# Performance work log

Measured on AMD Instinct MI355X. Metric: run time of the kernel, lower is better.

## Reference

```python
import jax, jax.numpy as jnp
import numpy as np
import math

VOCAB = 2048
SEQ = 2048
BATCH = 8
NEG_INF = -1e30


def setup_inputs() -> dict:
    key = jax.random.key(0)
    ks = jax.random.split(key, 8)
    sV = 1.0 / math.sqrt(VOCAB)
    sS = 1.0 / math.sqrt(SEQ)
    return {
        "input": jax.random.randint(ks[0], (BATCH, SEQ), 0, VOCAB),
        "emb": jax.random.normal(ks[1], (VOCAB, VOCAB), jnp.float32),   # nn.Embedding(vocab, vocab)
        "pos": jax.random.normal(ks[2], (SEQ, SEQ), jnp.float32),       # nn.Embedding(seq, seq)
        "WQ1": jax.random.normal(ks[3], (SEQ, SEQ), jnp.float32) * sS,  # Linear(seq, seq), (out,in)
        "WK1": jax.random.normal(ks[4], (SEQ, SEQ), jnp.float32) * sS,
        "WV1": jax.random.normal(ks[5], (VOCAB, VOCAB), jnp.float32) * sV,
        "WQ2": jax.random.normal(ks[6], (VOCAB, VOCAB), jnp.float32) * sV,
        "WK2": jax.random.normal(ks[7], (VOCAB, VOCAB), jnp.float32) * sV,
        "beta_1": jnp.float32(1.0),
        "beta_2": jnp.float32(1.0),
        "beta_out": jnp.float32(1.0),
    }


def reference(input, emb, pos, WQ1, WK1, WV1, WQ2, WK2, beta_1, beta_2, beta_out):
    S, V = SEQ, VOCAB
    E = emb[input]                       # (B, S, V)
    P = pos                              # positions(arange(S)) == full table, (S, S)

    # --- stage 1: batch-independent causal attention over positions ---
    Q1 = P @ WQ1.T                       # (S, S)
    K1 = P @ WK1.T                       # (S, S)
    S1 = beta_1 * (Q1 @ K1.T) / math.sqrt(S)
    causal = jnp.tril(jnp.ones((S, S), bool))
    S1 = jnp.where(causal, S1, NEG_INF)
    A1 = jax.nn.softmax(S1, axis=-1)
    A1 = A1.at[0, :].set(0.0)            # zero first query row (per-batch identical)

    V1 = jnp.einsum('bsv,wv->bsw', E, WV1)   # WV1(E), (B, S, V)
    Y1 = jnp.einsum('st,btv->bsv', A1, V1)
    Z1 = E + Y1                          # (B, S, V)

    # --- stage 2: single-query attention ---
    q2 = Z1[:, -1] @ WQ2.T               # (B, V)
    K2 = jnp.einsum('bsv,wv->bsw', Z1, WK2)  # (B, S, V)
    S2 = beta_2 * jnp.einsum('bv,bsv->bs', q2, K2) / math.sqrt(V)  # (B, S)
    last_two = jnp.arange(S) >= S - 2
    S2 = jnp.where(last_two[None, :], NEG_INF, S2)
    A2 = jax.nn.softmax(S2, axis=-1)     # (B, S)

    Y2 = jnp.einsum('bs,bsv->bv', A2, E)
    return beta_out * Y2                 # (B, V) == output[:, 0, :]
```

## Files before the change

kernel.cpp:

```cpp
#include <hip/hip_runtime.h>
#include <math.h>

#define SEQ 2048
#define VOCAB 2048
#define BATCH 8
#define NTRIL 136

typedef unsigned short u16;
typedef __attribute__((ext_vector_type(4))) float f32x4;
typedef __attribute__((ext_vector_type(8))) short bf16x8;

__device__ __forceinline__ u16 f2bf(float f) {
  unsigned int u = __builtin_bit_cast(unsigned int, f);
  u += 0x7fffu + ((u >> 16) & 1u);
  return (u16)(u >> 16);
}

__device__ __forceinline__ float b2f(u16 h) {
  unsigned int u = ((unsigned int)h) << 16;
  return __builtin_bit_cast(float, u);
}

__device__ __forceinline__ void async16(const void* g, void* l) {
  __builtin_amdgcn_global_load_lds((const __attribute__((address_space(1))) void*)g,
                                   (__attribute__((address_space(3))) void*)l, 16, 0, 0);
}

__global__ __launch_bounds__(256) void cvt_all(const float* __restrict__ pos, const float* __restrict__ WQ1,
                                               const float* __restrict__ WK1, u16* __restrict__ Pbf,
                                               u16* __restrict__ Wqk, float4* __restrict__ zreg, int nz4) {
  const int i = blockIdx.x * 256 + threadIdx.x;
  const int seg = blockIdx.y;
  if (seg == 3) {
    if (i < nz4) zreg[i] = make_float4(0.f, 0.f, 0.f, 0.f);
    return;
  }
  const float* src = (seg == 0) ? pos : (seg == 1) ? WQ1 : WK1;
  u16* dst = (seg == 0) ? Pbf : (seg == 1) ? Wqk : Wqk + (size_t)SEQ * SEQ;
  float4 v = ((const float4*)src)[i];
  ushort4 o;
  o.x = f2bf(v.x); o.y = f2bf(v.y); o.z = f2bf(v.z); o.w = f2bf(v.w);
  ((ushort4*)dst)[i] = o;
}

__device__ __forceinline__ void stage_tile(const u16* __restrict__ A, const u16* __restrict__ B,
                                           u16* As, u16* Bs, int m0, int n0, int kt,
                                           int wid, int lane) {
  const int c0 = wid * 2;
  const int skel = (lane & 3) * 8;
#pragma unroll
  for (int r = 0; r < 2; ++r) {
    const int chunk = c0 + r;
    const int row = chunk * 16 + (lane >> 2);
    async16(A + (size_t)(m0 + row) * SEQ + kt + skel, As + chunk * 512);
    async16(B + (size_t)(n0 + row) * SEQ + kt + skel, Bs + chunk * 512);
  }
}

__device__ __forceinline__ void compute_tile(const u16* As, const u16* Bs, f32x4 acc[4][4],
                                             int wr, int wc, int frow, int fk) {
  bf16x8 af[4], bfv[4];
#pragma unroll
  for (int mi = 0; mi < 4; ++mi) af[mi] = *(const bf16x8*)&As[(wr * 64 + mi * 16 + frow) * 32 + fk];
#pragma unroll
  for (int ni = 0; ni < 4; ++ni) bfv[ni] = *(const bf16x8*)&Bs[(wc * 64 + ni * 16 + frow) * 32 + fk];
#pragma unroll
  for (int mi = 0; mi < 4; ++mi)
#pragma unroll
    for (int ni = 0; ni < 4; ++ni)
      acc[mi][ni] = __builtin_amdgcn_mfma_f32_16x16x32_bf16(af[mi], bfv[ni], acc[mi][ni], 0, 0, 0);
}

__global__ __launch_bounds__(256) void gemm_qk(const u16* __restrict__ A, const u16* __restrict__ Bw,
                                               u16* __restrict__ Q1b, u16* __restrict__ K1b) {
  __shared__ __align__(16) u16 As0[4096], Bs0[4096], As1[4096], Bs1[4096];
  const int bid = blockIdx.x;
  const int xcd = bid & 7, li = bid >> 3;
  const int tx = (xcd & 3) * 8 + (li & 7);
  const int ty = (xcd >> 2) * 8 + (li >> 3);
  const int m0 = ty * 128;
  const int n0 = tx * 128;

  const int tid = threadIdx.x;
  const int wid = tid >> 6;
  const int lane = tid & 63;
  const int wr = wid >> 1, wc = wid & 1;
  const int frow = lane & 15;
  const int fk = (lane >> 4) * 8;

  f32x4 acc[4][4];
#pragma unroll
  for (int i = 0; i < 4; ++i)
#pragma unroll
    for (int j = 0; j < 4; ++j) acc[i][j] = (f32x4){0.f, 0.f, 0.f, 0.f};

  stage_tile(A, Bw, As0, Bs0, m0, n0, 0, wid, lane);
  __syncthreads();
  const int NT = SEQ / 32;
  for (int t = 0; t < NT - 1; t += 2) {
    stage_tile(A, Bw, As1, Bs1, m0, n0, (t + 1) * 32, wid, lane);
    compute_tile(As0, Bs0, acc, wr, wc, frow, fk);
    __syncthreads();
    if (t + 2 < NT) stage_tile(A, Bw, As0, Bs0, m0, n0, (t + 2) * 32, wid, lane);
    compute_tile(As1, Bs1, acc, wr, wc, frow, fk);
    __syncthreads();
  }

  u16* outp = (n0 < SEQ) ? Q1b : K1b;
  const int rbase = m0 + wr * 64;
  const int cbase = (n0 < SEQ ? n0 : n0 - SEQ) + wc * 64;
  const int rl = (lane >> 4) * 4;
  const int cl = lane & 15;
#pragma unroll
  for (int mi = 0; mi < 4; ++mi)
#pragma unroll
    for (int ni = 0; ni < 4; ++ni)
#pragma unroll
      for (int i = 0; i < 4; ++i) {
        int rr = rbase + mi * 16 + rl + i;
        int cc = cbase + ni * 16 + cl;
        outp[(size_t)rr * SEQ + cc] = f2bf(acc[mi][ni][i]);
      }
}

__global__ __launch_bounds__(256) void gemm_s1(const u16* __restrict__ A, const u16* __restrict__ B,
                                               u16* __restrict__ part) {
  __shared__ __align__(16) u16 As0[4096], Bs0[4096], As1[4096], Bs1[4096];
  const int bid = blockIdx.x;
  const int split = bid & 3;
  const int t = bid >> 2;
  int ti_m = 0;
  while (((ti_m + 1) * (ti_m + 2)) / 2 <= t) ++ti_m;
  const int ti_n = t - (ti_m * (ti_m + 1)) / 2;
  const int m0 = ti_m * 128;
  const int n0 = ti_n * 128;
  const int kt0 = split * (SEQ / 4);

  const int tid = threadIdx.x;
  const int wid = tid >> 6;
  const int lane = tid & 63;
  const int wr = wid >> 1, wc = wid & 1;
  const int frow = lane & 15;
  const int fk = (lane >> 4) * 8;

  f32x4 acc[4][4];
#pragma unroll
  for (int i = 0; i < 4; ++i)
#pragma unroll
    for (int j = 0; j < 4; ++j) acc[i][j] = (f32x4){0.f, 0.f, 0.f, 0.f};

  stage_tile(A, B, As0, Bs0, m0, n0, kt0, wid, lane);
  __syncthreads();
  const int NT = (SEQ / 4) / 32;
  for (int tt = 0; tt < NT - 1; tt += 2) {
    stage_tile(A, B, As1, Bs1, m0, n0, kt0 + (tt + 1) * 32, wid, lane);
    compute_tile(As0, Bs0, acc, wr, wc, frow, fk);
    __syncthreads();
    if (tt + 2 < NT) stage_tile(A, B, As0, Bs0, m0, n0, kt0 + (tt + 2) * 32, wid, lane);
    compute_tile(As1, Bs1, acc, wr, wc, frow, fk);
    __syncthreads();
  }

  u16* dst = part + ((size_t)(split * NTRIL + t) << 14);
  const int rb = wr * 64;
  const int cb = wc * 64;
  const int rl = (lane >> 4) * 4;
  const int cl = lane & 15;
#pragma unroll
  for (int mi = 0; mi < 4; ++mi)
#pragma unroll
    for (int ni = 0; ni < 4; ++ni)
#pragma unroll
      for (int i = 0; i < 4; ++i)
        dst[(rb + mi * 16 + rl + i) * 128 + (cb + ni * 16 + cl)] = f2bf(acc[mi][ni][i]);
}

__global__ __launch_bounds__(256) void softmax_last(const u16* __restrict__ part, const float* __restrict__ b1p,
                                                    const int* __restrict__ idx, float* __restrict__ cnt1) {
  const int b = blockIdx.x;
  const int tid = threadIdx.x, lane = tid & 63, w = tid >> 6;
  __shared__ float buf[SEQ];
  __shared__ float red[8];
  const float c1 = b1p[0] / sqrtf((float)SEQ);
  const int base_t = 120;
  const u16* p0 = part + ((size_t)(0 * NTRIL + base_t) << 14) + 127 * 128;
  const u16* p1 = part + ((size_t)(1 * NTRIL + base_t) << 14) + 127 * 128;
  const u16* p2 = part + ((size_t)(2 * NTRIL + base_t) << 14) + 127 * 128;
  const u16* p3 = part + ((size_t)(3 * NTRIL + base_t) << 14) + 127 * 128;
  float mx = -3.0e38f;
  for (int q = tid; q < SEQ / 4; q += 256) {
    const size_t o = ((size_t)(q >> 5) << 14) + ((q << 2) & 127);
    ushort4 a0 = *(const ushort4*)(p0 + o);
    ushort4 a1 = *(const ushort4*)(p1 + o);
    ushort4 a2 = *(const ushort4*)(p2 + o);
    ushort4 a3 = *(const ushort4*)(p3 + o);
    float v0 = (b2f(a0.x) + b2f(a1.x) + b2f(a2.x) + b2f(a3.x)) * c1;
    float v1 = (b2f(a0.y) + b2f(a1.y) + b2f(a2.y) + b2f(a3.y)) * c1;
    float v2 = (b2f(a0.z) + b2f(a1.z) + b2f(a2.z) + b2f(a3.z)) * c1;
    float v3 = (b2f(a0.w) + b2f(a1.w) + b2f(a2.w) + b2f(a3.w)) * c1;
    const int j = q << 2;
    buf[j] = v0; buf[j + 1] = v1; buf[j + 2] = v2; buf[j + 3] = v3;
    mx = fmaxf(mx, fmaxf(fmaxf(v0, v1), fmaxf(v2, v3)));
  }
  for (int o = 32; o > 0; o >>= 1) mx = fmaxf(mx, __shfl_down(mx, o));
  if (lane == 0) red[w] = mx;
  __syncthreads();
  if (tid == 0) { float m = red[0]; for (int i = 1; i < 4; ++i) m = fmaxf(m, red[i]); red[4] = m; }
  __syncthreads();
  const float MX = red[4];
  float sm = 0.f;
  for (int j = tid; j < SEQ; j += 256) {
    float e = expf(buf[j] - MX);
    buf[j] = e;
    sm += e;
  }
  for (int o = 32; o > 0; o >>= 1) sm += __shfl_down(sm, o);
  if (lane == 0) red[w] = sm;
  __syncthreads();
  if (tid == 0) { float tt = 0.f; for (int i = 0; i < 4; ++i) tt += red[i]; red[5] = tt; }
  __syncthreads();
  const float inv = 1.0f / red[5];
  for (int j = tid; j < SEQ; j += 256)
    atomicAdd(&cnt1[b * VOCAB + idx[b * SEQ + j]], buf[j] * inv);
}

__global__ __launch_bounds__(256) void matvec_col(const float* __restrict__ M, const float* __restrict__ x,
                                                  float* __restrict__ outp, const float* __restrict__ scale_ptr) {
  const int vb = blockIdx.x * 256 + threadIdx.x;
  const int w0 = blockIdx.y * 32;
  __shared__ float xs[BATCH][32];
  { int k = threadIdx.x; xs[k >> 5][k & 31] = x[(k >> 5) * VOCAB + w0 + (k & 31)]; }
  __syncthreads();
  float acc[BATCH];
#pragma unroll
  for (int b = 0; b < BATCH; ++b) acc[b] = 0.f;
#pragma unroll 8
  for (int j = 0; j < 32; ++j) {
    float m = M[(size_t)(w0 + j) * VOCAB + vb];
#pragma unroll
    for (int b = 0; b < BATCH; ++b) acc[b] += xs[b][j] * m;
  }
  float sc = scale_ptr ? scale_ptr[0] : 1.0f;
#pragma unroll
  for (int b = 0; b < BATCH; ++b) atomicAdd(&outp[b * VOCAB + vb], sc * acc[b]);
}

template<int GATHER_ADD>
__global__ __launch_bounds__(256) void matvec_row(const float* __restrict__ M, const float* __restrict__ x,
                                                  float* __restrict__ outp, const int* __restrict__ idx,
                                                  const float* __restrict__ emb) {
  const int lane = threadIdx.x & 63;
  const int i = blockIdx.x * 4 + (threadIdx.x >> 6);
  const float4* m4 = (const float4*)(M + (size_t)i * VOCAB);
  const float4* x4 = (const float4*)x;
  float acc[BATCH];
#pragma unroll
  for (int b = 0; b < BATCH; ++b) acc[b] = 0.f;
  for (int v = lane; v < VOCAB / 4; v += 64) {
    float4 m = m4[v];
#pragma unroll
    for (int b = 0; b < BATCH; ++b) {
      float4 xv = x4[b * (VOCAB / 4) + v];
      acc[b] += m.x * xv.x + m.y * xv.y + m.z * xv.z + m.w * xv.w;
    }
  }
#pragma unroll
  for (int b = 0; b < BATCH; ++b)
    for (int o = 32; o > 0; o >>= 1) acc[b] += __shfl_down(acc[b], o);
  if (lane == 0) {
#pragma unroll
    for (int b = 0; b < BATCH; ++b) {
      float s = acc[b];
      if (GATHER_ADD) s += emb[(size_t)idx[b * SEQ + SEQ - 1] * VOCAB + i];
      outp[b * VOCAB + i] = s;
    }
  }
}

__global__ __launch_bounds__(256) void emb_dots16(const float* __restrict__ emb, const float* __restrict__ rw,
                                                  float* __restrict__ D) {
  const int lane = threadIdx.x & 63;
  const int i = blockIdx.x * 4 + (threadIdx.x >> 6);
  const float4* e4 = (const float4*)(emb + (size_t)i * VOCAB);
  const float4* r4 = (const float4*)rw;
  float acc[16];
#pragma unroll
  for (int j = 0; j < 16; ++j) acc[j] = 0.f;
  for (int v = lane; v < VOCAB / 4; v += 64) {
    float4 m = e4[v];
#pragma unroll
    for (int j = 0; j < 16; ++j) {
      float4 r = r4[j * (VOCAB / 4) + v];
      acc[j] += m.x * r.x + m.y * r.y + m.z * r.z + m.w * r.w;
    }
  }
#pragma unroll
  for (int j = 0; j < 16; ++j)
    for (int o = 32; o > 0; o >>= 1) acc[j] += __shfl_down(acc[j], o);
  if (lane == 0) {
#pragma unroll
    for (int j = 0; j < 16; ++j) D[(size_t)i * 16 + j] = acc[j];
  }
}

__global__ __launch_bounds__(256) void gath_u(const int* __restrict__ idx, const float* __restrict__ D,
                                              float* __restrict__ u) {
  const int i = blockIdx.x * 256 + threadIdx.x;
  const int b = i >> 11;
  u[i] = D[(size_t)idx[i] * 16 + 8 + b];
}

__global__ __launch_bounds__(256) void sm_apply(const u16* __restrict__ part, const float* __restrict__ b1p,
                                                const float* __restrict__ u, float* __restrict__ vv) {
  const int s = blockIdx.x;
  const int tid = threadIdx.x, lane = tid & 63, w = tid >> 6;
  if (s == 0) {
    if (tid < BATCH) vv[tid * SEQ] = 0.f;
    return;
  }
  __shared__ float buf[SEQ];
  __shared__ float red[8];
  __shared__ float red2[4][BATCH];
  const float c1 = b1p[0] / sqrtf((float)SEQ);
  const int base_t = (s >> 7) * ((s >> 7) + 1) / 2;
  const int rloc = (s & 127) * 128;
  const u16* p0 = part + ((size_t)(0 * NTRIL + base_t) << 14) + rloc;
  const u16* p1 = part + ((size_t)(1 * NTRIL + base_t) << 14) + rloc;
  const u16* p2 = part + ((size_t)(2 * NTRIL + base_t) << 14) + rloc;
  const u16* p3 = part + ((size_t)(3 * NTRIL + base_t) << 14) + rloc;
  float mx = -3.0e38f;
  const int nq = (s + 1) >> 2;
  for (int q = tid; q < nq; q += 256) {
    const size_t o = ((size_t)(q >> 5) << 14) + ((q << 2) & 127);
    ushort4 a0 = *(const ushort4*)(p0 + o);
    ushort4 a1 = *(const ushort4*)(p1 + o);
    ushort4 a2 = *(const ushort4*)(p2 + o);
    ushort4 a3 = *(const ushort4*)(p3 + o);
    float v0 = (b2f(a0.x) + b2f(a1.x) + b2f(a2.x) + b2f(a3.x)) * c1;
    float v1 = (b2f(a0.y) + b2f(a1.y) + b2f(a2.y) + b2f(a3.y)) * c1;
    float v2 = (b2f(a0.z) + b2f(a1.z) + b2f(a2.z) + b2f(a3.z)) * c1;
    float v3 = (b2f(a0.w) + b2f(a1.w) + b2f(a2.w) + b2f(a3.w)) * c1;
    const int j = q << 2;
    buf[j] = v0; buf[j + 1] = v1; buf[j + 2] = v2; buf[j + 3] = v3;
    mx = fmaxf(mx, fmaxf(fmaxf(v0, v1), fmaxf(v2, v3)));
  }
  {
    const int j = (nq << 2) + tid;
    if (j <= s) {
      const size_t o = ((size_t)(j >> 7) << 14) + (j & 127);
      float v = (b2f(p0[o]) + b2f(p1[o]) + b2f(p2[o]) + b2f(p3[o])) * c1;
      buf[j] = v;
      mx = fmaxf(mx, v);
    }
  }
  for (int o = 32; o > 0; o >>= 1) mx = fmaxf(mx, __shfl_down(mx, o));
  if (lane == 0) red[w] = mx;
  __syncthreads();
  if (tid == 0) { float m = red[0]; for (int i = 1; i < 4; ++i) m = fmaxf(m, red[i]); red[4] = m; }
  __syncthreads();
  const float MX = red[4];
  float sm = 0.f;
  for (int j = tid; j <= s; j += 256) {
    float e = expf(buf[j] - MX);
    buf[j] = e;
    sm += e;
  }
  for (int o = 32; o > 0; o >>= 1) sm += __shfl_down(sm, o);
  if (lane == 0) red[w] = sm;
  __syncthreads();
  if (tid == 0) { float tt = 0.f; for (int i = 0; i < 4; ++i) tt += red[i]; red[5] = tt; }
  __syncthreads();
  const float inv = 1.0f / red[5];
  float acc[BATCH];
#pragma unroll
  for (int b = 0; b < BATCH; ++b) acc[b] = 0.f;
  for (int q = tid; q < nq; q += 256) {
    const int j = q << 2;
    float4 a = *(float4*)&buf[j];
#pragma unroll
    for (int b = 0; b < BATCH; ++b) {
      float4 uv = *(const float4*)(u + b * SEQ + j);
      acc[b] += a.x * uv.x + a.y * uv.y + a.z * uv.z + a.w * uv.w;
    }
  }
  {
    const int j = (nq << 2) + tid;
    if (j <= s) {
      float a = buf[j];
#pragma unroll
      for (int b = 0; b < BATCH; ++b) acc[b] += a * u[b * SEQ + j];
    }
  }
#pragma unroll
  for (int b = 0; b < BATCH; ++b)
    for (int o = 32; o > 0; o >>= 1) acc[b] += __shfl_down(acc[b], o);
  if (lane == 0)
#pragma unroll
    for (int b = 0; b < BATCH; ++b) red2[w][b] = acc[b];
  __syncthreads();
  if (tid < BATCH)
    vv[tid * SEQ + s] = (red2[0][tid] + red2[1][tid] + red2[2][tid] + red2[3][tid]) * inv;
}

__global__ __launch_bounds__(256) void softmax2(const float* __restrict__ D, const float* __restrict__ vv,
                                                const int* __restrict__ idx, float* __restrict__ cnt2,
                                                const float* __restrict__ b2p, float4* __restrict__ out_zero) {
  const int b = blockIdx.x;
  const int tid = threadIdx.x, lane = tid & 63, w = tid >> 6;
  for (int k = b * 256 + tid; k < BATCH * VOCAB / 4; k += BATCH * 256)
    out_zero[k] = make_float4(0.f, 0.f, 0.f, 0.f);
  __shared__ float buf[SEQ];
  __shared__ float red[8];
  const float c2 = b2p[0] / sqrtf((float)VOCAB);
  for (int s = tid; s < SEQ; s += 256) {
    float val = -1.0e30f;
    if (s < SEQ - 2) {
      float ee = D[(size_t)idx[b * SEQ + s] * 16 + b];
      val = c2 * (ee + vv[b * SEQ + s]);
    }
    buf[s] = val;
  }
  __syncthreads();
  float mx = -3.0e38f;
  for (int s = tid; s < SEQ; s += 256) mx = fmaxf(mx, buf[s]);
  for (int o = 32; o > 0; o >>= 1) mx = fmaxf(mx, __shfl_down(mx, o));
  if (lane == 0) red[w] = mx;
  __syncthreads();
  if (tid == 0) { float m = red[0]; for (int i = 1; i < 4; ++i) m = fmaxf(m, red[i]); red[4] = m; }
  __syncthreads();
  const float MX = red[4];
  float sm = 0.f;
  for (int s = tid; s < SEQ; s += 256) {
    float e = expf(buf[s] - MX);
    buf[s] = e;
    sm += e;
  }
  for (int o = 32; o > 0; o >>= 1) sm += __shfl_down(sm, o);
  if (lane == 0) red[w] = sm;
  __syncthreads();
  if (tid == 0) { float tt = 0.f; for (int i = 0; i < 4; ++i) tt += red[i]; red[5] = tt; }
  __syncthreads();
  const float inv = 1.0f / red[5];
  for (int s = tid; s < SEQ - 2; s += 256)
    atomicAdd(&cnt2[b * VOCAB + idx[b * SEQ + s]], buf[s] * inv);
}

extern "C" void kernel_launch(void* const* d_in, const int* in_sizes, int n_in,
                              void* d_out, int out_size, void* d_ws, size_t ws_size,
                              hipStream_t stream) {
  (void)in_sizes; (void)n_in; (void)out_size; (void)ws_size;
  const int*   idx = (const int*)d_in[0];
  const float* emb = (const float*)d_in[1];
  const float* pos = (const float*)d_in[2];
  const float* WQ1 = (const float*)d_in[3];
  const float* WK1 = (const float*)d_in[4];
  const float* WV1 = (const float*)d_in[5];
  const float* WQ2 = (const float*)d_in[6];
  const float* WK2 = (const float*)d_in[7];
  const float* b1  = (const float*)d_in[8];
  const float* b2  = (const float*)d_in[9];
  const float* bo  = (const float*)d_in[10];
  float* out = (float*)d_out;

  size_t off = 0;
  auto take = [&](size_t n) { void* p = (char*)d_ws + off; off += (n + 255) & ~(size_t)255; return p; };
  u16*   Pbf  = (u16*)take((size_t)SEQ * SEQ * 2);
  u16*   Wqk  = (u16*)take((size_t)SEQ * SEQ * 4);
  u16*   Q1b  = (u16*)take((size_t)SEQ * SEQ * 2);
  u16*   K1b  = (u16*)take((size_t)SEQ * SEQ * 2);
  u16*   S1p  = (u16*)take((size_t)4 * NTRIL * 16384 * 2);
  float* g    = (float*)take((size_t)BATCH * VOCAB * 4);
  float* cnt1 = (float*)take((size_t)BATCH * VOCAB * 4);
  float* rr   = (float*)take((size_t)BATCH * VOCAB * 4);
  float* wv   = (float*)take((size_t)BATCH * VOCAB * 4);
  float* cnt2 = (float*)take((size_t)BATCH * VOCAB * 4);
  float* zl   = (float*)take((size_t)BATCH * VOCAB * 4);
  float* q2   = (float*)take((size_t)BATCH * VOCAB * 4);
  float* D    = (float*)take((size_t)VOCAB * 16 * 4);
  float* uu   = (float*)take((size_t)BATCH * SEQ * 4);
  float* vv   = (float*)take((size_t)BATCH * SEQ * 4);
  (void)wv;

  const int nz4 = 5 * BATCH * VOCAB / 4;

  cvt_all<<<dim3(SEQ * SEQ / 4 / 256, 4), 256, 0, stream>>>(pos, WQ1, WK1, Pbf, Wqk, (float4*)g, nz4);

  gemm_qk<<<512, 256, 0, stream>>>(Pbf, Wqk, Q1b, K1b);

  gemm_s1<<<4 * NTRIL, 256, 0, stream>>>(Q1b, K1b, S1p);

  softmax_last<<<BATCH, 256, 0, stream>>>(S1p, b1, idx, cnt1);

  matvec_col<<<dim3(VOCAB / 256, 64), 256, 0, stream>>>(emb, cnt1, g, nullptr);

  matvec_row<1><<<VOCAB / 4, 256, 0, stream>>>(WV1, g, zl, idx, emb);
  matvec_row<0><<<VOCAB / 4, 256, 0, stream>>>(WQ2, zl, q2, nullptr, nullptr);

  matvec_col<<<dim3(VOCAB / 256, 64), 256, 0, stream>>>(WK2, q2, rr, nullptr);
  matvec_col<<<dim3(VOCAB / 256, 64), 256, 0, stream>>>(WV1, rr, wv, nullptr);

  emb_dots16<<<VOCAB / 4, 256, 0, stream>>>(emb, rr, D);

  gath_u<<<BATCH * SEQ / 256, 256, 0, stream>>>(idx, D, uu);

  sm_apply<<<SEQ, 256, 0, stream>>>(S1p, b1, uu, vv);

  softmax2<<<BATCH, 256, 0, stream>>>(D, vv, idx, cnt2, b2, (float4*)out);

  matvec_col<<<dim3(VOCAB / 256, 64), 256, 0, stream>>>(emb, cnt2, out, bo);
}
```

Baseline: 162.4 us.

## Deepen GEMM K-tile to 64 and compute four emb rows per wave

The two bf16 GEMMs now stage and compute 64-wide K slices per double-buffer step instead of 32, which halves the number of barriers and loop iterations and doubles LDS use per block. emb_dots16 now has each wave process four embedding rows, so every rw vector loaded is reused four times, and the grid shrinks to a quarter. The risks are lower occupancy from the larger LDS footprint, the 64-entry accumulator array raising register pressure, and far fewer blocks in emb_dots16.

```diff
diff --git a/kernel.cpp b/kernel.cpp
--- a/kernel.cpp
+++ b/kernel.cpp
@@ -43,37 +43,45 @@
   ((ushort4*)dst)[i] = o;
 }
 
-__device__ __forceinline__ void stage_tile(const u16* __restrict__ A, const u16* __restrict__ B,
-                                           u16* As, u16* Bs, int m0, int n0, int kt,
-                                           int wid, int lane) {
+__device__ __forceinline__ void stage64(const u16* __restrict__ A, const u16* __restrict__ B,
+                                        u16* As, u16* Bs, int m0, int n0, int kt,
+                                        int wid, int lane) {
   const int c0 = wid * 2;
   const int skel = (lane & 3) * 8;
 #pragma unroll
   for (int r = 0; r < 2; ++r) {
     const int chunk = c0 + r;
     const int row = chunk * 16 + (lane >> 2);
-    async16(A + (size_t)(m0 + row) * SEQ + kt + skel, As + chunk * 512);
-    async16(B + (size_t)(n0 + row) * SEQ + kt + skel, Bs + chunk * 512);
-  }
-}
-
-__device__ __forceinline__ void compute_tile(const u16* As, const u16* Bs, f32x4 acc[4][4],
-                                             int wr, int wc, int frow, int fk) {
-  bf16x8 af[4], bfv[4];
-#pragma unroll
-  for (int mi = 0; mi < 4; ++mi) af[mi] = *(const bf16x8*)&As[(wr * 64 + mi * 16 + frow) * 32 + fk];
-#pragma unroll
-  for (int ni = 0; ni < 4; ++ni) bfv[ni] = *(const bf16x8*)&Bs[(wc * 64 + ni * 16 + frow) * 32 + fk];
-#pragma unroll
-  for (int mi = 0; mi < 4; ++mi)
-#pragma unroll
-    for (int ni = 0; ni < 4; ++ni)
-      acc[mi][ni] = __builtin_amdgcn_mfma_f32_16x16x32_bf16(af[mi], bfv[ni], acc[mi][ni], 0, 0, 0);
+#pragma unroll
+    for (int kk = 0; kk < 2; ++kk) {
+      async16(A + (size_t)(m0 + row) * SEQ + kt + kk * 32 + skel, As + kk * 4096 + chunk * 512);
+      async16(B + (size_t)(n0 + row) * SEQ + kt + kk * 32 + skel, Bs + kk * 4096 + chunk * 512);
+    }
+  }
+}
+
+__device__ __forceinline__ void compute64(const u16* As, const u16* Bs, f32x4 acc[4][4],
+                                          int wr, int wc, int frow, int fk) {
+#pragma unroll
+  for (int kk = 0; kk < 2; ++kk) {
+    const u16* Ap = As + kk * 4096;
+    const u16* Bp = Bs + kk * 4096;
+    bf16x8 af[4], bfv[4];
+#pragma unroll
+    for (int mi = 0; mi < 4; ++mi) af[mi] = *(const bf16x8*)&Ap[(wr * 64 + mi * 16 + frow) * 32 + fk];
+#pragma unroll
+    for (int ni = 0; ni < 4; ++ni) bfv[ni] = *(const bf16x8*)&Bp[(wc * 64 + ni * 16 + frow) * 32 + fk];
+#pragma unroll
+    for (int mi = 0; mi < 4; ++mi)
+#pragma unroll
+      for (int ni = 0; ni < 4; ++ni)
+        acc[mi][ni] = __builtin_amdgcn_mfma_f32_16x16x32_bf16(af[mi], bfv[ni], acc[mi][ni], 0, 0, 0);
+  }
 }
 
 __global__ __launch_bounds__(256) void gemm_qk(const u16* __restrict__ A, const u16* __restrict__ Bw,
                                                u16* __restrict__ Q1b, u16* __restrict__ K1b) {
-  __shared__ __align__(16) u16 As0[4096], Bs0[4096], As1[4096], Bs1[4096];
+  __shared__ __align__(16) u16 As0[8192], Bs0[8192], As1[8192], Bs1[8192];
   const int bid = blockIdx.x;
   const int xcd = bid & 7, li = bid >> 3;
   const int tx = (xcd & 3) * 8 + (li & 7);
@@ -94,15 +102,15 @@
 #pragma unroll
     for (int j = 0; j < 4; ++j) acc[i][j] = (f32x4){0.f, 0.f, 0.f, 0.f};
 
-  stage_tile(A, Bw, As0, Bs0, m0, n0, 0, wid, lane);
-  __syncthreads();
-  const int NT = SEQ / 32;
+  stage64(A, Bw, As0, Bs0, m0, n0, 0, wid, lane);
+  __syncthreads();
+  const int NT = SEQ / 64;
   for (int t = 0; t < NT - 1; t += 2) {
-    stage_tile(A, Bw, As1, Bs1, m0, n0, (t + 1) * 32, wid, lane);
-    compute_tile(As0, Bs0, acc, wr, wc, frow, fk);
+    stage64(A, Bw, As1, Bs1, m0, n0, (t + 1) * 64, wid, lane);
+    compute64(As0, Bs0, acc, wr, wc, frow, fk);
     __syncthreads();
-    if (t + 2 < NT) stage_tile(A, Bw, As0, Bs0, m0, n0, (t + 2) * 32, wid, lane);
-    compute_tile(As1, Bs1, acc, wr, wc, frow, fk);
+    if (t + 2 < NT) stage64(A, Bw, As0, Bs0, m0, n0, (t + 2) * 64, wid, lane);
+    compute64(As1, Bs1, acc, wr, wc, frow, fk);
     __syncthreads();
   }
 
@@ -125,7 +133,7 @@
 
 __global__ __launch_bounds__(256) void gemm_s1(const u16* __restrict__ A, const u16* __restrict__ B,
                                                u16* __restrict__ part) {
-  __shared__ __align__(16) u16 As0[4096], Bs0[4096], As1[4096], Bs1[4096];
+  __shared__ __align__(16) u16 As0[8192], Bs0[8192], As1[8192], Bs1[8192];
   const int bid = blockIdx.x;
   const int split = bid & 3;
   const int t = bid >> 2;
@@ -149,15 +157,15 @@
 #pragma unroll
     for (int j = 0; j < 4; ++j) acc[i][j] = (f32x4){0.f, 0.f, 0.f, 0.f};
 
-  stage_tile(A, B, As0, Bs0, m0, n0, kt0, wid, lane);
-  __syncthreads();
-  const int NT = (SEQ / 4) / 32;
+  stage64(A, B, As0, Bs0, m0, n0, kt0, wid, lane);
+  __syncthreads();
+  const int NT = (SEQ / 4) / 64;
   for (int tt = 0; tt < NT - 1; tt += 2) {
-    stage_tile(A, B, As1, Bs1, m0, n0, kt0 + (tt + 1) * 32, wid, lane);
-    compute_tile(As0, Bs0, acc, wr, wc, frow, fk);
+    stage64(A, B, As1, Bs1, m0, n0, kt0 + (tt + 1) * 64, wid, lane);
+    compute64(As0, Bs0, acc, wr, wc, frow, fk);
     __syncthreads();
-    if (tt + 2 < NT) stage_tile(A, B, As0, Bs0, m0, n0, kt0 + (tt + 2) * 32, wid, lane);
-    compute_tile(As1, Bs1, acc, wr, wc, frow, fk);
+    if (tt + 2 < NT) stage64(A, B, As0, Bs0, m0, n0, kt0 + (tt + 2) * 64, wid, lane);
+    compute64(As1, Bs1, acc, wr, wc, frow, fk);
     __syncthreads();
   }
 
@@ -280,26 +288,39 @@
 __global__ __launch_bounds__(256) void emb_dots16(const float* __restrict__ emb, const float* __restrict__ rw,
                                                   float* __restrict__ D) {
   const int lane = threadIdx.x & 63;
-  const int i = blockIdx.x * 4 + (threadIdx.x >> 6);
-  const float4* e4 = (const float4*)(emb + (size_t)i * VOCAB);
+  const int wv = threadIdx.x >> 6;
+  const int i0 = (blockIdx.x * 4 + wv) * 4;
+  const float4* e4 = (const float4*)(emb + (size_t)i0 * VOCAB);
   const float4* r4 = (const float4*)rw;
-  float acc[16];
-#pragma unroll
-  for (int j = 0; j < 16; ++j) acc[j] = 0.f;
+  float acc[4][16];
+#pragma unroll
+  for (int wi = 0; wi < 4; ++wi)
+#pragma unroll
+    for (int j = 0; j < 16; ++j) acc[wi][j] = 0.f;
   for (int v = lane; v < VOCAB / 4; v += 64) {
-    float4 m = e4[v];
+    float4 m0 = e4[v];
+    float4 m1 = e4[512 + v];
+    float4 m2 = e4[1024 + v];
+    float4 m3 = e4[1536 + v];
 #pragma unroll
     for (int j = 0; j < 16; ++j) {
-      float4 r = r4[j * (VOCAB / 4) + v];
-      acc[j] += m.x * r.x + m.y * r.y + m.z * r.z + m.w * r.w;
-    }
-  }
-#pragma unroll
-  for (int j = 0; j < 16; ++j)
-    for (int o = 32; o > 0; o >>= 1) acc[j] += __shfl_down(acc[j], o);
+      float4 r = r4[j * 512 + v];
+      acc[0][j] += m0.x * r.x + m0.y * r.y + m0.z * r.z + m0.w * r.w;
+      acc[1][j] += m1.x * r.x + m1.y * r.y + m1.z * r.z + m1.w * r.w;
+      acc[2][j] += m2.x * r.x + m2.y * r.y + m2.z * r.z + m2.w * r.w;
+      acc[3][j] += m3.x * r.x + m3.y * r.y + m3.z * r.z + m3.w * r.w;
+    }
+  }
+#pragma unroll
+  for (int wi = 0; wi < 4; ++wi)
+#pragma unroll
+    for (int j = 0; j < 16; ++j)
+      for (int o = 32; o > 0; o >>= 1) acc[wi][j] += __shfl_down(acc[wi][j], o);
   if (lane == 0) {
 #pragma unroll
-    for (int j = 0; j < 16; ++j) D[(size_t)i * 16 + j] = acc[j];
+    for (int wi = 0; wi < 4; ++wi)
+#pragma unroll
+      for (int j = 0; j < 16; ++j) D[(size_t)(i0 + wi) * 16 + j] = acc[wi][j];
   }
 }
 
@@ -499,7 +520,7 @@
   matvec_col<<<dim3(VOCAB / 256, 64), 256, 0, stream>>>(WK2, q2, rr, nullptr);
   matvec_col<<<dim3(VOCAB / 256, 64), 256, 0, stream>>>(WV1, rr, wv, nullptr);
 
-  emb_dots16<<<VOCAB / 4, 256, 0, stream>>>(emb, rr, D);
+  emb_dots16<<<VOCAB / 16, 256, 0, stream>>>(emb, rr, D);
 
   gath_u<<<BATCH * SEQ / 256, 256, 0, stream>>>(idx, D, uu);
 
```

After: 191.2 us. 17.8% more time.
